# Performance work log

Measured on AMD Instinct MI355X. Metric: run time of the kernel, lower is better.

## Reference

```python
import jax, jax.numpy as jnp
import numpy as np


def setup_inputs() -> dict:
    key = jax.random.key(0)
    ks = jax.random.split(key, 8)
    B, N, H = 8, 64, 256
    nE, E = 256, 64
    HID, OUT = 512, 1
    s1 = 1.0 / np.sqrt(H + E)
    s2 = 1.0 / np.sqrt(HID)
    return {
        "h_all": jax.random.normal(ks[0], (B, N, H), dtype=jnp.float32),
        "e_feat": jax.random.normal(ks[1], (nE, E), dtype=jnp.float32),
        "W1": jax.random.normal(ks[2], (H + E, HID), dtype=jnp.float32) * s1,
        "b1": jnp.zeros((HID,), dtype=jnp.float32),
        "W2": jax.random.normal(ks[3], (HID, HID), dtype=jnp.float32) * s2,
        "b2": jnp.zeros((HID,), dtype=jnp.float32),
        "W3": jax.random.normal(ks[4], (HID, OUT), dtype=jnp.float32) * s2,
        "b3": jnp.zeros((OUT,), dtype=jnp.float32),
    }


def reference(h_all, e_feat, W1, b1, W2, b2, W3, b3):
    # Math == MLP(cat([expand(h), expand(e)], -1)) but computed via split
    # weights: cat([h,e]) @ W1 == h @ W1[:H] + e @ W1[H:], avoiding the
    # materialized [B,N,nE,H+E] concat tensor.
    H = h_all.shape[-1]
    Wh, We = W1[:H], W1[H:]
    h_part = jnp.einsum("bnh,hk->bnk", h_all, Wh)        # [B,N,HID]
    e_part = jnp.einsum("ed,dk->ek", e_feat, We)          # [nE,HID]
    x = h_part[:, :, None, :] + e_part[None, None, :, :] + b1  # [B,N,nE,HID]
    x = jax.nn.relu(x)
    x = jax.nn.relu(jnp.einsum("bnek,kj->bnej", x, W2) + b2)
    return jnp.einsum("bnek,ko->bneo", x, W3) + b3        # [B,N,nE,OUT]
```

## Files before the change

kernel.cpp:

```cpp
#include <hip/hip_runtime.h>
#include <hip/hip_bf16.h>


typedef __attribute__((ext_vector_type(8))) short bf16x8;
typedef __attribute__((ext_vector_type(4))) float f32x4;

static __device__ __forceinline__ ushort2 pk_bf16(float a, float b) {
  union { __hip_bfloat162 h; ushort2 u; } c;
  c.h = __float22bfloat162_rn(make_float2(a, b));
  return c.u;
}

__global__ __launch_bounds__(256) void k_prep(
    const float* __restrict__ h_all, const float* __restrict__ e_feat,
    const float* __restrict__ W1, const float* __restrict__ b1,
    const float* __restrict__ W2,
    float* __restrict__ hpb, float* __restrict__ ep,
    unsigned short* __restrict__ w2f) {
  __shared__ float sm[64 * 68];
  const int t = threadIdx.x;
  const int b = blockIdx.x;

  if (b < 64) {
    const int r0 = b * 8;
    float (*hs)[256] = (float(*)[256])sm;
    #pragma unroll
    for (int i = 0; i < 8; ++i) hs[i][t] = h_all[(size_t)(r0 + i) * 256 + t];
    __syncthreads();
    float2 acc[8];
    #pragma unroll
    for (int i = 0; i < 8; ++i) acc[i] = make_float2(0.f, 0.f);
    for (int k = 0; k < 256; ++k) {
      float2 wv = *(const float2*)(W1 + (size_t)k * 512 + 2 * t);
      #pragma unroll
      for (int i = 0; i < 8; ++i) {
        acc[i].x = fmaf(hs[i][k], wv.x, acc[i].x);
        acc[i].y = fmaf(hs[i][k], wv.y, acc[i].y);
      }
    }
    float2 bv = *(const float2*)(b1 + 2 * t);
    #pragma unroll
    for (int i = 0; i < 8; ++i) {
      float2 o = make_float2(acc[i].x + bv.x, acc[i].y + bv.y);
      *(float2*)(hpb + (size_t)(r0 + i) * 512 + 2 * t) = o;
    }
  } else if (b < 96) {
    const int r0 = (b - 64) * 8;
    sm[t] = e_feat[(size_t)r0 * 64 + t];
    sm[256 + t] = e_feat[(size_t)r0 * 64 + 256 + t];
    __syncthreads();
    float2 acc[8];
    #pragma unroll
    for (int i = 0; i < 8; ++i) acc[i] = make_float2(0.f, 0.f);
    for (int k = 0; k < 64; ++k) {
      float2 wv = *(const float2*)(W1 + (size_t)(256 + k) * 512 + 2 * t);
      #pragma unroll
      for (int i = 0; i < 8; ++i) {
        acc[i].x = fmaf(sm[i * 64 + k], wv.x, acc[i].x);
        acc[i].y = fmaf(sm[i * 64 + k], wv.y, acc[i].y);
      }
    }
    #pragma unroll
    for (int i = 0; i < 8; ++i)
      *(float2*)(ep + (size_t)(r0 + i) * 512 + 2 * t) =
          make_float2(acc[i].x, acc[i].y);
  } else {
    const int bb = b - 96;
    const int k0 = (bb >> 3) * 64;
    const int c0 = (bb & 7) * 64;
    #pragma unroll
    for (int rr = 0; rr < 4; ++rr) {
      const int row = rr * 16 + (t >> 4);
      float4 v = *(const float4*)(W2 + (size_t)(k0 + row) * 512 + c0 + (t & 15) * 4);
      *(float4*)(&sm[row * 68 + (t & 15) * 4]) = v;
    }
    __syncthreads();
    #pragma unroll
    for (int s2 = 0; s2 < 2; ++s2) {
      const int s = t * 2 + s2;
      const int rec = s >> 6, l = s & 63;
      const int jg = (c0 >> 4) + (rec & 3);
      const int ksg = (k0 >> 5) + (rec >> 2);
      const int cl = (rec & 3) * 16 + (l & 15);
      const int kl = (rec >> 2) * 32 + (l >> 4) * 8;
      union { ushort2 o[4]; uint4 v; } u;
      #pragma unroll
      for (int uu = 0; uu < 4; ++uu)
        u.o[uu] = pk_bf16(sm[(kl + 2 * uu) * 68 + cl], sm[(kl + 2 * uu + 1) * 68 + cl]);
      *(uint4*)(w2f + ((size_t)(jg * 16 + ksg) * 64 + l) * 8) = u.v;
    }
  }
}

__global__ __launch_bounds__(256, 2) void k_main(
    const float* __restrict__ hpb, const float* __restrict__ ep,
    const unsigned short* __restrict__ w2f, const float* __restrict__ b2,
    const float* __restrict__ W3, const float* __restrict__ b3,
    float* __restrict__ out) {
  __shared__ unsigned short x1s[64 * 512];

  const int t = threadIdx.x;
  const int lane = t & 63;
  const int w = t >> 6;
  const int l15 = lane & 15, l4 = lane >> 4;
  const int bn = blockIdx.x >> 2;
  const int e0 = (blockIdx.x & 3) << 6;
  const float* hprow = hpb + (size_t)bn * 512;

  {
    const int kk = (t & 127) * 4;
    const int rbase = t >> 7;
    const int ch = kk >> 3;
    const int kin = kk & 7;
    const float4 hv = *(const float4*)(hprow + kk);
    #pragma unroll 4
    for (int rr = 0; rr < 32; ++rr) {
      const int r = rr * 2 + rbase;
      float4 ev = *(const float4*)(ep + (size_t)(e0 + r) * 512 + kk);
      ushort2 p0 = pk_bf16(fmaxf(ev.x + hv.x, 0.f), fmaxf(ev.y + hv.y, 0.f));
      ushort2 p1 = pk_bf16(fmaxf(ev.z + hv.z, 0.f), fmaxf(ev.w + hv.w, 0.f));
      ushort4 pk4 = {p0.x, p0.y, p1.x, p1.y};
      *(ushort4*)(&x1s[r * 512 + (ch ^ (r & 7)) * 8 + kin]) = pk4;
    }
  }

  const unsigned short* wrec = w2f + (size_t)w * 65536 + (size_t)lane * 8;
  bf16x8 bcur[8], bnxt[8];
  #pragma unroll
  for (int j = 0; j < 8; ++j)
    bcur[j] = *(const bf16x8*)(wrec + j * 8192);
  __syncthreads();

  f32x4 acc[4][8] = {};
  #pragma unroll 2
  for (int ks = 0; ks < 16; ++ks) {
    const int ksn = (ks + 1) & 15;
    const int chp = (((ks * 4 + l4) ^ (l15 & 7)) * 8);
    bf16x8 a[4];
    #pragma unroll
    for (int i = 0; i < 4; ++i)
      a[i] = *(const bf16x8*)(&x1s[(i * 16 + l15) * 512 + chp]);
    #pragma unroll
    for (int j = 0; j < 8; ++j)
      bnxt[j] = *(const bf16x8*)(wrec + j * 8192 + ksn * 512);
    #pragma unroll
    for (int i = 0; i < 4; ++i)
      #pragma unroll
      for (int j = 0; j < 8; ++j)
        acc[i][j] = __builtin_amdgcn_mfma_f32_16x16x32_bf16(a[i], bcur[j], acc[i][j], 0, 0, 0);
    #pragma unroll
    for (int j = 0; j < 8; ++j) bcur[j] = bnxt[j];
  }

  float part[16];
  #pragma unroll
  for (int u = 0; u < 16; ++u) part[u] = 0.f;
  #pragma unroll
  for (int j = 0; j < 8; ++j) {
    const int n = w * 128 + j * 16 + l15;
    const float b2v = b2[n], w3v = W3[n];
    #pragma unroll
    for (int i = 0; i < 4; ++i)
      #pragma unroll
      for (int r = 0; r < 4; ++r)
        part[i * 4 + r] = fmaf(fmaxf(acc[i][j][r] + b2v, 0.f), w3v, part[i * 4 + r]);
  }
  #pragma unroll
  for (int u = 0; u < 16; ++u) {
    float v = part[u];
    v += __shfl_xor(v, 1);
    v += __shfl_xor(v, 2);
    v += __shfl_xor(v, 4);
    v += __shfl_xor(v, 8);
    part[u] = v;
  }
  __syncthreads();
  float* osum = (float*)x1s;
  if (l15 == 0) {
    #pragma unroll
    for (int i = 0; i < 4; ++i)
      #pragma unroll
      for (int r = 0; r < 4; ++r)
        osum[w * 64 + i * 16 + l4 * 4 + r] = part[i * 4 + r];
  }
  __syncthreads();
  if (t < 64) {
    float s = b3[0] + osum[t] + osum[64 + t] + osum[128 + t] + osum[192 + t];
    out[(size_t)blockIdx.x * 64 + t] = s;
  }
}

extern "C" void kernel_launch(void* const* d_in, const int* in_sizes, int n_in,
                              void* d_out, int out_size, void* d_ws, size_t ws_size,
                              hipStream_t stream) {
  const float* h_all  = (const float*)d_in[0];
  const float* e_feat = (const float*)d_in[1];
  const float* W1     = (const float*)d_in[2];
  const float* b1     = (const float*)d_in[3];
  const float* W2     = (const float*)d_in[4];
  const float* b2     = (const float*)d_in[5];
  const float* W3     = (const float*)d_in[6];
  const float* b3     = (const float*)d_in[7];
  float* out = (float*)d_out;

  float* hpb = (float*)d_ws;
  float* ep = hpb + 512 * 512;
  unsigned short* w2f = (unsigned short*)(ep + 256 * 512);

  hipLaunchKernelGGL(k_prep, dim3(160), dim3(256), 0, stream,
                     h_all, e_feat, W1, b1, W2, hpb, ep, w2f);
  hipLaunchKernelGGL(k_main, dim3(2048), dim3(256), 0, stream,
                     hpb, ep, w2f, b2, W3, b3, out);
}
```

Measured before the change: 154.2 us.

## Double e-rows per block in main kernel and store e-projection as bf16

```diff
diff --git a/kernel.cpp b/kernel.cpp
--- a/kernel.cpp
+++ b/kernel.cpp
@@ -10,42 +10,51 @@
   c.h = __float22bfloat162_rn(make_float2(a, b));
   return c.u;
 }
+static __device__ __forceinline__ float bf2f(unsigned short u) {
+  union { unsigned int i; float f; } c;
+  c.i = ((unsigned int)u) << 16;
+  return c.f;
+}
 
 __global__ __launch_bounds__(256) void k_prep(
     const float* __restrict__ h_all, const float* __restrict__ e_feat,
     const float* __restrict__ W1, const float* __restrict__ b1,
     const float* __restrict__ W2,
-    float* __restrict__ hpb, float* __restrict__ ep,
+    float* __restrict__ hpb, unsigned short* __restrict__ epb,
     unsigned short* __restrict__ w2f) {
   __shared__ float sm[64 * 68];
   const int t = threadIdx.x;
   const int b = blockIdx.x;
 
-  if (b < 64) {
-    const int r0 = b * 8;
+  if (b < 256) {
+    const int r0 = b * 2;
     float (*hs)[256] = (float(*)[256])sm;
-    #pragma unroll
-    for (int i = 0; i < 8; ++i) hs[i][t] = h_all[(size_t)(r0 + i) * 256 + t];
+    hs[0][t] = h_all[(size_t)r0 * 256 + t];
+    hs[1][t] = h_all[(size_t)(r0 + 1) * 256 + t];
     __syncthreads();
-    float2 acc[8];
-    #pragma unroll
-    for (int i = 0; i < 8; ++i) acc[i] = make_float2(0.f, 0.f);
-    for (int k = 0; k < 256; ++k) {
-      float2 wv = *(const float2*)(W1 + (size_t)k * 512 + 2 * t);
-      #pragma unroll
-      for (int i = 0; i < 8; ++i) {
-        acc[i].x = fmaf(hs[i][k], wv.x, acc[i].x);
-        acc[i].y = fmaf(hs[i][k], wv.y, acc[i].y);
-      }
+    float2 a0 = make_float2(0.f, 0.f), a1 = make_float2(0.f, 0.f);
+    #pragma unroll 2
+    for (int k = 0; k < 256; k += 4) {
+      float2 w0 = *(const float2*)(W1 + (size_t)k * 512 + 2 * t);
+      float2 w1 = *(const float2*)(W1 + (size_t)(k + 1) * 512 + 2 * t);
+      float2 w2v = *(const float2*)(W1 + (size_t)(k + 2) * 512 + 2 * t);
+      float2 w3v = *(const float2*)(W1 + (size_t)(k + 3) * 512 + 2 * t);
+      float h00 = hs[0][k], h01 = hs[0][k + 1], h02 = hs[0][k + 2], h03 = hs[0][k + 3];
+      float h10 = hs[1][k], h11 = hs[1][k + 1], h12 = hs[1][k + 2], h13 = hs[1][k + 3];
+      a0.x = fmaf(h00, w0.x, a0.x); a0.y = fmaf(h00, w0.y, a0.y);
+      a1.x = fmaf(h10, w0.x, a1.x); a1.y = fmaf(h10, w0.y, a1.y);
+      a0.x = fmaf(h01, w1.x, a0.x); a0.y = fmaf(h01, w1.y, a0.y);
+      a1.x = fmaf(h11, w1.x, a1.x); a1.y = fmaf(h11, w1.y, a1.y);
+      a0.x = fmaf(h02, w2v.x, a0.x); a0.y = fmaf(h02, w2v.y, a0.y);
+      a1.x = fmaf(h12, w2v.x, a1.x); a1.y = fmaf(h12, w2v.y, a1.y);
+      a0.x = fmaf(h03, w3v.x, a0.x); a0.y = fmaf(h03, w3v.y, a0.y);
+      a1.x = fmaf(h13, w3v.x, a1.x); a1.y = fmaf(h13, w3v.y, a1.y);
     }
     float2 bv = *(const float2*)(b1 + 2 * t);
-    #pragma unroll
-    for (int i = 0; i < 8; ++i) {
-      float2 o = make_float2(acc[i].x + bv.x, acc[i].y + bv.y);
-      *(float2*)(hpb + (size_t)(r0 + i) * 512 + 2 * t) = o;
-    }
-  } else if (b < 96) {
-    const int r0 = (b - 64) * 8;
+    *(float2*)(hpb + (size_t)r0 * 512 + 2 * t) = make_float2(a0.x + bv.x, a0.y + bv.y);
+    *(float2*)(hpb + (size_t)(r0 + 1) * 512 + 2 * t) = make_float2(a1.x + bv.x, a1.y + bv.y);
+  } else if (b < 288) {
+    const int r0 = (b - 256) * 8;
     sm[t] = e_feat[(size_t)r0 * 64 + t];
     sm[256 + t] = e_feat[(size_t)r0 * 64 + 256 + t];
     __syncthreads();
@@ -62,10 +71,9 @@
     }
     #pragma unroll
     for (int i = 0; i < 8; ++i)
-      *(float2*)(ep + (size_t)(r0 + i) * 512 + 2 * t) =
-          make_float2(acc[i].x, acc[i].y);
+      *(ushort2*)(epb + (size_t)(r0 + i) * 512 + 2 * t) = pk_bf16(acc[i].x, acc[i].y);
   } else {
-    const int bb = b - 96;
+    const int bb = b - 288;
     const int k0 = (bb >> 3) * 64;
     const int c0 = (bb & 7) * 64;
     #pragma unroll
@@ -92,20 +100,28 @@
   }
 }
 
-__global__ __launch_bounds__(256, 2) void k_main(
-    const float* __restrict__ hpb, const float* __restrict__ ep,
+__global__ __launch_bounds__(512, 2) void k_main(
+    const float* __restrict__ hpb, const unsigned short* __restrict__ epb,
     const unsigned short* __restrict__ w2f, const float* __restrict__ b2,
     const float* __restrict__ W3, const float* __restrict__ b3,
     float* __restrict__ out) {
-  __shared__ unsigned short x1s[64 * 512];
+  __shared__ unsigned short x1s[128 * 512];
 
   const int t = threadIdx.x;
   const int lane = t & 63;
   const int w = t >> 6;
+  const int wc = w & 3;
+  const int wrh = w >> 2;
   const int l15 = lane & 15, l4 = lane >> 4;
-  const int bn = blockIdx.x >> 2;
-  const int e0 = (blockIdx.x & 3) << 6;
+  const int bn = blockIdx.x >> 1;
+  const int e0 = (blockIdx.x & 1) << 7;
   const float* hprow = hpb + (size_t)bn * 512;
+
+  const unsigned short* wrec = w2f + (size_t)wc * 65536 + (size_t)lane * 8;
+  bf16x8 bcur[8], bnxt[8];
+  #pragma unroll
+  for (int j = 0; j < 8; ++j)
+    bcur[j] = *(const bf16x8*)(wrec + j * 8192);
 
   {
     const int kk = (t & 127) * 4;
@@ -115,31 +131,27 @@
     const float4 hv = *(const float4*)(hprow + kk);
     #pragma unroll 4
     for (int rr = 0; rr < 32; ++rr) {
-      const int r = rr * 2 + rbase;
-      float4 ev = *(const float4*)(ep + (size_t)(e0 + r) * 512 + kk);
-      ushort2 p0 = pk_bf16(fmaxf(ev.x + hv.x, 0.f), fmaxf(ev.y + hv.y, 0.f));
-      ushort2 p1 = pk_bf16(fmaxf(ev.z + hv.z, 0.f), fmaxf(ev.w + hv.w, 0.f));
+      const int r = rr * 4 + rbase;
+      ushort4 ev = *(const ushort4*)(epb + (size_t)(e0 + r) * 512 + kk);
+      ushort2 p0 = pk_bf16(fmaxf(bf2f(ev.x) + hv.x, 0.f), fmaxf(bf2f(ev.y) + hv.y, 0.f));
+      ushort2 p1 = pk_bf16(fmaxf(bf2f(ev.z) + hv.z, 0.f), fmaxf(bf2f(ev.w) + hv.w, 0.f));
       ushort4 pk4 = {p0.x, p0.y, p1.x, p1.y};
       *(ushort4*)(&x1s[r * 512 + (ch ^ (r & 7)) * 8 + kin]) = pk4;
     }
   }
-
-  const unsigned short* wrec = w2f + (size_t)w * 65536 + (size_t)lane * 8;
-  bf16x8 bcur[8], bnxt[8];
-  #pragma unroll
-  for (int j = 0; j < 8; ++j)
-    bcur[j] = *(const bf16x8*)(wrec + j * 8192);
   __syncthreads();
 
   f32x4 acc[4][8] = {};
   #pragma unroll 2
   for (int ks = 0; ks < 16; ++ks) {
     const int ksn = (ks + 1) & 15;
-    const int chp = (((ks * 4 + l4) ^ (l15 & 7)) * 8);
     bf16x8 a[4];
     #pragma unroll
-    for (int i = 0; i < 4; ++i)
-      a[i] = *(const bf16x8*)(&x1s[(i * 16 + l15) * 512 + chp]);
+    for (int i = 0; i < 4; ++i) {
+      const int r = wrh * 64 + i * 16 + l15;
+      const int chp = (((ks * 4 + l4) ^ (l15 & 7)) * 8);
+      a[i] = *(const bf16x8*)(&x1s[r * 512 + chp]);
+    }
     #pragma unroll
     for (int j = 0; j < 8; ++j)
       bnxt[j] = *(const bf16x8*)(wrec + j * 8192 + ksn * 512);
@@ -157,7 +169,7 @@
   for (int u = 0; u < 16; ++u) part[u] = 0.f;
   #pragma unroll
   for (int j = 0; j < 8; ++j) {
-    const int n = w * 128 + j * 16 + l15;
+    const int n = wc * 128 + j * 16 + l15;
     const float b2v = b2[n], w3v = W3[n];
     #pragma unroll
     for (int i = 0; i < 4; ++i)
@@ -181,12 +193,12 @@
     for (int i = 0; i < 4; ++i)
       #pragma unroll
       for (int r = 0; r < 4; ++r)
-        osum[w * 64 + i * 16 + l4 * 4 + r] = part[i * 4 + r];
+        osum[wc * 128 + wrh * 64 + i * 16 + l4 * 4 + r] = part[i * 4 + r];
   }
   __syncthreads();
-  if (t < 64) {
-    float s = b3[0] + osum[t] + osum[64 + t] + osum[128 + t] + osum[192 + t];
-    out[(size_t)blockIdx.x * 64 + t] = s;
+  if (t < 128) {
+    float s = b3[0] + osum[t] + osum[128 + t] + osum[256 + t] + osum[384 + t];
+    out[(size_t)bn * 256 + e0 + t] = s;
   }
 }
 
@@ -204,11 +216,11 @@
   float* out = (float*)d_out;
 
   float* hpb = (float*)d_ws;
-  float* ep = hpb + 512 * 512;
-  unsigned short* w2f = (unsigned short*)(ep + 256 * 512);
-
-  hipLaunchKernelGGL(k_prep, dim3(160), dim3(256), 0, stream,
-                     h_all, e_feat, W1, b1, W2, hpb, ep, w2f);
-  hipLaunchKernelGGL(k_main, dim3(2048), dim3(256), 0, stream,
-                     hpb, ep, w2f, b2, W3, b3, out);
-}
+  unsigned short* epb = (unsigned short*)(hpb + 512 * 512);
+  unsigned short* w2f = epb + 256 * 512;
+
+  hipLaunchKernelGGL(k_prep, dim3(352), dim3(256), 0, stream,
+                     h_all, e_feat, W1, b1, W2, hpb, epb, w2f);
+  hipLaunchKernelGGL(k_main, dim3(1024), dim3(512), 0, stream,
+                     hpb, epb, w2f, b2, W3, b3, out);
+}
```

Result: no change. 152.9 us (-0.9%).
